# Kernel tuning notes

Measured on AMD Instinct MI355X. Metric: run time of the kernel, lower is better.

## Reference

```python
import jax, jax.numpy as jnp
import numpy as np

FRS = np.array([1, 2, 4, 8, 16, 25, 36, 50, 75], dtype=np.float32)
N_EXPERTS = len(FRS)
N = 1048576
DIMS = [(4, 32), (32, 32), (32, 64), (64, 64)]


def setup_inputs() -> dict:
    key = jax.random.key(0)
    ks = jax.random.split(key, 2 + 8)
    # features: col 0 = framerate drawn from the known framerate set, cols 1:5 = affinity feats
    fr_idx = jax.random.randint(ks[0], (N,), 0, N_EXPERTS)
    framerates = jnp.asarray(FRS)[fr_idx]
    aff = jax.random.normal(ks[1], (N, 4), dtype=jnp.float32)
    features = jnp.concatenate([framerates[:, None], aff], axis=1)
    # stacked per-expert MLP params (torch Linear: y = x @ W.T + b; store W as [in,out])
    params = {}
    scale = 0.1
    for li, (din, dout) in enumerate(DIMS):
        params[f"W{li+1}"] = scale * jax.random.normal(ks[2 + 2 * li], (N_EXPERTS, din, dout), dtype=jnp.float32)
        params[f"b{li+1}"] = scale * jax.random.normal(ks[3 + 2 * li], (N_EXPERTS, dout), dtype=jnp.float32)
    return {"features": features, **params}


def _expert_mlp(x, W1, b1, W2, b2, W3, b3, W4, b4):
    h = jax.nn.relu(x @ W1 + b1)
    h = jax.nn.relu(h @ W2 + b2)
    h = jax.nn.relu(h @ W3 + b3)
    return h @ W4 + b4  # [N, 64]


def reference(features, W1, b1, W2, b2, W3, b3, W4, b4):
    frs = jnp.asarray(FRS)
    framerates = features[:, 0]
    x = features[:, 1:]  # [N, 4] (ignore_appr=False)
    # nearest-framerate expert index (argmin picks first min, matching find_index)
    k = jnp.argmin(jnp.abs(framerates[:, None] - frs[None, :]), axis=1)  # [N]
    pred = jnp.zeros(features.shape[0], dtype=features.dtype)
    for e in range(N_EXPERTS):  # fixed, small expert set
        out_e = _expert_mlp(x, W1[e], b1[e], W2[e], b2[e], W3[e], b3[e], W4[e], b4[e])
        pred = jnp.where(k == e, out_e.sum(axis=1), pred)
    return pred
```

## Files before the change

### kernel.cpp

```cpp
#include <hip/hip_runtime.h>
#include <stdint.h>

#define NEXP 9
#define FTHR 512
#define RPH 4
#define SBLK (FTHR * RPH)
#define PADSLK (SBLK + NEXP * 32)
#define MAXT 80
#define TBL_BYTES 7936
#define CLS_STRIDE 168

typedef float f32x4 __attribute__((ext_vector_type(4)));
typedef float f32x16 __attribute__((ext_vector_type(16)));
typedef _Float16 f16x8 __attribute__((ext_vector_type(8)));

struct alignas(16) I4 { int a, b, c, d; };
struct alignas(64) Q4 { f32x4 a, b, c, d; };

__device__ __forceinline__ int pk(float a, float b) {
    return __builtin_bit_cast(int, __builtin_amdgcn_cvt_pkrtz(a, b));
}
__device__ __forceinline__ f32x16 zero16() {
    f32x16 z;
#pragma unroll
    for (int r = 0; r < 16; ++r) z[r] = 0.f;
    return z;
}

__device__ __forceinline__ int expert_of(float fr) {
    const float frs[NEXP] = {1.f, 2.f, 4.f, 8.f, 16.f, 25.f, 36.f, 50.f, 75.f};
    int k = 0;
    float best = fabsf(fr - frs[0]);
#pragma unroll
    for (int e = 1; e < NEXP; ++e) {
        float d = fabsf(fr - frs[e]);
        if (d < best) { best = d; k = e; }
    }
    return k;
}

__global__ __launch_bounds__(256) void k_prep(const float* __restrict__ W1, const float* __restrict__ b1,
                                              const float* __restrict__ W2, const float* __restrict__ b2,
                                              const float* __restrict__ W3, const float* __restrict__ b3,
                                              const float* __restrict__ W4, const float* __restrict__ b4,
                                              char* __restrict__ tab) {
    int e = blockIdx.x;
    int tid = threadIdx.x;
    char* T = tab + (size_t)e * TBL_BYTES;

    __shared__ float psum[64][4];
    __shared__ float rs2[64];
    __shared__ float b4s_s;
    {
        int row = tid >> 2, q = tid & 3;
        const float* w = W4 + (size_t)e * 4096 + row * 64 + q * 16;
        f32x4 a = *(const f32x4*)(w + 0), b = *(const f32x4*)(w + 4);
        f32x4 c = *(const f32x4*)(w + 8), d = *(const f32x4*)(w + 12);
        psum[row][q] = (a.x + a.y + a.z + a.w) + (b.x + b.y + b.z + b.w)
                     + (c.x + c.y + c.z + c.w) + (d.x + d.y + d.z + d.w);
    }
    __syncthreads();
    if (tid < 64) {
        int l = tid, g = l >> 5, m = l & 31;
        rs2[l] = psum[l][0] + psum[l][1] + psum[l][2] + psum[l][3];
        float bp = b4[e * 64 + l];
#pragma unroll
        for (int d = 1; d < 64; d <<= 1) bp += __shfl_xor(bp, d, 64);
        if (l == 0) b4s_s = bp;

        {
            f16x8 v;
#pragma unroll
            for (int ei = 0; ei < 8; ++ei) {
                int k = g * 8 + ei;
                float w = (k < 4) ? W1[e * 128 + k * 32 + m] : (k == 4 ? b1[e * 32 + m] : 0.f);
                v[ei] = (_Float16)w;
            }
            *(f16x8*)(T + 0 * 1024 + l * 16) = v;
        }
#pragma unroll
        for (int kf = 0; kf < 2; ++kf) {
            f16x8 v;
#pragma unroll
            for (int ei = 0; ei < 8; ++ei) {
                int row = kf * 16 + (ei & 3) + 8 * (ei >> 2) + 4 * g;
                v[ei] = (_Float16)W2[e * 1024 + row * 32 + m];
            }
            *(f16x8*)(T + (1 + kf) * 1024 + l * 16) = v;
        }
#pragma unroll
        for (int t = 0; t < 2; ++t)
#pragma unroll
            for (int kf = 0; kf < 2; ++kf) {
                f16x8 v;
#pragma unroll
                for (int ei = 0; ei < 8; ++ei) {
                    int row = kf * 16 + (ei & 3) + 8 * (ei >> 2) + 4 * g;
                    v[ei] = (_Float16)W3[e * 2048 + row * 64 + t * 32 + m];
                }
                *(f16x8*)(T + (3 + t * 2 + kf) * 1024 + l * 16) = v;
            }
    }
    __syncthreads();
    if (tid < 32) {
        int g = tid >> 4, r = tid & 15;
        int row = (r & 3) + 8 * (r >> 2) + 4 * g;
        float* C = (float*)(T + 7168);
        C[0 * 32 + tid] = b2[e * 32 + row];
        C[1 * 32 + tid] = b3[e * 64 + row];
        C[2 * 32 + tid] = b3[e * 64 + 32 + row];
        C[3 * 32 + tid] = rs2[row];
        C[4 * 32 + tid] = rs2[32 + row];
        if (tid == 0) C[160] = b4s_s;
    }
}

__global__ __launch_bounds__(FTHR, 4) void k_main(const float* __restrict__ feat, int n,
                                                  const char* __restrict__ tab,
                                                  float* __restrict__ out) {
    __shared__ uint2 bx[PADSLK];
    __shared__ unsigned short bidx[PADSLK];
    __shared__ float cls[NEXP * CLS_STRIDE];
    __shared__ int lcnt[NEXP];
    __shared__ int pbase[NEXP];
    __shared__ int wbase[RPH][8][NEXP];
    __shared__ unsigned char tile_e[MAXT];
    __shared__ short tile_s[MAXT];
    __shared__ unsigned char tile_v[MAXT];
    __shared__ int nt_s;

    int bid = blockIdx.x, tid = threadIdx.x;
    int wid = tid >> 6, lane = tid & 63, g = lane >> 5, m = lane & 31;
    int gbase = bid * SBLK;

    if (tid < NEXP) lcnt[tid] = 0;
    {
        uint2 z = {0u, 0u};
#pragma unroll
        for (int q = 0; q < 5; ++q) {
            int o = q * FTHR + tid;
            if (o < PADSLK) bx[o] = z;
        }
    }
    {
        const float* tf = (const float*)tab;
        for (int idx = tid; idx < NEXP * 161; idx += FTHR) {
            int e = idx / 161, o = idx - e * 161;
            cls[e * CLS_STRIDE + o] = tf[e * (TBL_BYTES / 4) + 1792 + o];
        }
    }
    __syncthreads();

    int kk[RPH], rk[RPH];
    uint2 xw[RPH];
#pragma unroll
    for (int r = 0; r < RPH; ++r) {
        int i = gbase + r * FTHR + tid;
        int k = -1;
        uint2 w = {0u, 0u};
        if (i < n) {
            const float* f = feat + (size_t)i * 5;
            k = expert_of(f[0]);
            w.x = (unsigned)pk(f[1], f[2]);
            w.y = (unsigned)pk(f[3], f[4]);
        }
        kk[r] = k; xw[r] = w;
        unsigned long long myM = 0;
#pragma unroll
        for (int e = 0; e < NEXP; ++e) {
            unsigned long long mm = __ballot(k == e);
            if (k == e) myM = mm;
            if (lane == 0) {
                int c = __popcll(mm);
                wbase[r][wid][e] = c ? atomicAdd(&lcnt[e], c) : 0;
            }
        }
        rk[r] = __popcll(myM & ((1ull << lane) - 1ull));
    }
    __syncthreads();

    if (wid == 0) {
        int e = lane;
        int c = (e < NEXP) ? lcnt[e] : 0;
        int ntl = (c + 31) >> 5;
        int padc = ntl << 5;
        int sp = padc, st = ntl;
#pragma unroll
        for (int d = 1; d < 16; d <<= 1) {
            int a = __shfl_up(sp, d, 64);
            int b = __shfl_up(st, d, 64);
            if (lane >= d) { sp += a; st += b; }
        }
        if (e < NEXP) {
            int pb = sp - padc, tb = st - ntl;
            pbase[e] = pb;
            for (int j = 0; j < ntl; ++j) {
                tile_e[tb + j] = (unsigned char)e;
                tile_s[tb + j] = (short)(pb + j * 32);
                int v = c - j * 32;
                tile_v[tb + j] = (unsigned char)(v > 32 ? 32 : v);
            }
            if (e == NEXP - 1) nt_s = st;
        }
    }
    __syncthreads();

#pragma unroll
    for (int r = 0; r < RPH; ++r) {
        int k = kk[r];
        if (k >= 0) {
            int slot = pbase[k] + wbase[r][wid][k] + rk[r];
            bx[slot] = xw[r];
            bidx[slot] = (unsigned short)(r * FTHR + tid);
        }
    }
    __syncthreads();

    int nt = nt_s;
    int t0 = (wid * nt) >> 3, t1 = ((wid + 1) * nt) >> 3;
    int cur_e = -1;
    f16x8 A1 = {}, A2a = {}, A2b = {}, A30a = {}, A30b = {}, A31a = {}, A31b = {};
    f32x16 W40r = zero16(), W41r = zero16();
    float b4v = 0.f;
    const float* Cc = cls;
    for (int t = t0; t < t1; ++t) {
        int e = __builtin_amdgcn_readfirstlane((int)tile_e[t]);
        if (e != cur_e) {
            cur_e = e;
            const char* T = tab + (size_t)e * TBL_BYTES;
            A1 = *(const f16x8*)(T + 0 * 1024 + lane * 16);
            A2a = *(const f16x8*)(T + 1 * 1024 + lane * 16);
            A2b = *(const f16x8*)(T + 2 * 1024 + lane * 16);
            A30a = *(const f16x8*)(T + 3 * 1024 + lane * 16);
            A30b = *(const f16x8*)(T + 4 * 1024 + lane * 16);
            A31a = *(const f16x8*)(T + 5 * 1024 + lane * 16);
            A31b = *(const f16x8*)(T + 6 * 1024 + lane * 16);
            Cc = cls + e * CLS_STRIDE + g * 16;
            {
                Q4 q;
                const float* c = Cc + 3 * 32;
                q.a = *(const f32x4*)(c + 0); q.b = *(const f32x4*)(c + 4);
                q.c = *(const f32x4*)(c + 8); q.d = *(const f32x4*)(c + 12);
                W40r = __builtin_bit_cast(f32x16, q);
                const float* c2 = Cc + 4 * 32;
                q.a = *(const f32x4*)(c2 + 0); q.b = *(const f32x4*)(c2 + 4);
                q.c = *(const f32x4*)(c2 + 8); q.d = *(const f32x4*)(c2 + 12);
                W41r = __builtin_bit_cast(f32x16, q);
            }
            b4v = cls[e * CLS_STRIDE + 160];
        }
        auto ldC = [&](int mat) -> f32x16 {
            const float* c = Cc + mat * 32;
            Q4 q;
            q.a = *(const f32x4*)(c + 0);
            q.b = *(const f32x4*)(c + 4);
            q.c = *(const f32x4*)(c + 8);
            q.d = *(const f32x4*)(c + 12);
            return __builtin_bit_cast(f32x16, q);
        };

        int s = tile_s[t], v = tile_v[t];
        uint2 xv = bx[s + m];

        I4 b1i = {g ? 0 : (int)xv.x, g ? 0 : (int)xv.y, g ? 0 : 0x3C00, 0};
        f16x8 B1 = __builtin_bit_cast(f16x8, b1i);

        f32x16 d1 = __builtin_amdgcn_mfma_f32_32x32x16_f16(A1, B1, zero16(), 0, 0, 0);
#pragma unroll
        for (int r = 0; r < 16; ++r) d1[r] = fmaxf(d1[r], 0.f);
        I4 p0 = {pk(d1[0], d1[1]), pk(d1[2], d1[3]), pk(d1[4], d1[5]), pk(d1[6], d1[7])};
        I4 p1 = {pk(d1[8], d1[9]), pk(d1[10], d1[11]), pk(d1[12], d1[13]), pk(d1[14], d1[15])};
        f16x8 B2a = __builtin_bit_cast(f16x8, p0);
        f16x8 B2b = __builtin_bit_cast(f16x8, p1);

        f32x16 d2 = __builtin_amdgcn_mfma_f32_32x32x16_f16(A2a, B2a, ldC(0), 0, 0, 0);
        d2 = __builtin_amdgcn_mfma_f32_32x32x16_f16(A2b, B2b, d2, 0, 0, 0);
#pragma unroll
        for (int r = 0; r < 16; ++r) d2[r] = fmaxf(d2[r], 0.f);
        I4 q0 = {pk(d2[0], d2[1]), pk(d2[2], d2[3]), pk(d2[4], d2[5]), pk(d2[6], d2[7])};
        I4 q1 = {pk(d2[8], d2[9]), pk(d2[10], d2[11]), pk(d2[12], d2[13]), pk(d2[14], d2[15])};
        f16x8 B3a = __builtin_bit_cast(f16x8, q0);
        f16x8 B3b = __builtin_bit_cast(f16x8, q1);

        float acc = 0.f;
        {
            f32x16 d3 = __builtin_amdgcn_mfma_f32_32x32x16_f16(A30a, B3a, ldC(1), 0, 0, 0);
            d3 = __builtin_amdgcn_mfma_f32_32x32x16_f16(A30b, B3b, d3, 0, 0, 0);
#pragma unroll
            for (int r = 0; r < 16; ++r) acc += fmaxf(d3[r], 0.f) * W40r[r];
        }
        {
            f32x16 d3 = __builtin_amdgcn_mfma_f32_32x32x16_f16(A31a, B3a, ldC(2), 0, 0, 0);
            d3 = __builtin_amdgcn_mfma_f32_32x32x16_f16(A31b, B3b, d3, 0, 0, 0);
#pragma unroll
            for (int r = 0; r < 16; ++r) acc += fmaxf(d3[r], 0.f) * W41r[r];
        }
        acc += __shfl_xor(acc, 32, 64);
        float rres = acc + b4v;
        if (!g && m < v) out[gbase + (int)bidx[s + m]] = rres;
    }
}

__global__ __launch_bounds__(256) void k_fallback(const float* __restrict__ feat,
                                                  const float* __restrict__ W1, const float* __restrict__ b1,
                                                  const float* __restrict__ W2, const float* __restrict__ b2,
                                                  const float* __restrict__ W3, const float* __restrict__ b3,
                                                  const float* __restrict__ W4, const float* __restrict__ b4,
                                                  float* __restrict__ out, int n) {
    int i = blockIdx.x * 256 + threadIdx.x;
    if (i >= n) return;
    const float* f = feat + (size_t)i * 5;
    int e = expert_of(f[0]);
    float x0 = f[1], x1 = f[2], x2 = f[3], x3 = f[4];
    float h1[32], h2[32], h3[64];
    for (int j = 0; j < 32; ++j) {
        float a = b1[e * 32 + j];
        a += x0 * W1[e * 128 + 0 * 32 + j];
        a += x1 * W1[e * 128 + 1 * 32 + j];
        a += x2 * W1[e * 128 + 2 * 32 + j];
        a += x3 * W1[e * 128 + 3 * 32 + j];
        h1[j] = fmaxf(a, 0.f);
    }
    for (int j = 0; j < 32; ++j) h2[j] = b2[e * 32 + j];
    for (int i2 = 0; i2 < 32; ++i2)
        for (int j = 0; j < 32; ++j) h2[j] += h1[i2] * W2[e * 1024 + i2 * 32 + j];
    for (int j = 0; j < 32; ++j) h2[j] = fmaxf(h2[j], 0.f);
    for (int j = 0; j < 64; ++j) h3[j] = b3[e * 64 + j];
    for (int i2 = 0; i2 < 32; ++i2)
        for (int j = 0; j < 64; ++j) h3[j] += h2[i2] * W3[e * 2048 + i2 * 64 + j];
    float pred = 0.f;
    for (int o = 0; o < 64; ++o) pred += b4[e * 64 + o];
    for (int j = 0; j < 64; ++j) {
        float rsum = 0.f;
        for (int o = 0; o < 64; ++o) rsum += W4[e * 4096 + j * 64 + o];
        pred += fmaxf(h3[j], 0.f) * rsum;
    }
    out[i] = pred;
}

extern "C" void kernel_launch(void* const* d_in, const int* in_sizes, int n_in,
                              void* d_out, int out_size, void* d_ws, size_t ws_size,
                              hipStream_t stream) {
    const float* feat = (const float*)d_in[0];
    const float* W1 = (const float*)d_in[1];
    const float* b1 = (const float*)d_in[2];
    const float* W2 = (const float*)d_in[3];
    const float* b2 = (const float*)d_in[4];
    const float* W3 = (const float*)d_in[5];
    const float* b3 = (const float*)d_in[6];
    const float* W4 = (const float*)d_in[7];
    const float* b4 = (const float*)d_in[8];
    float* out = (float*)d_out;
    int n = in_sizes[0] / 5;

    const size_t need = (size_t)NEXP * TBL_BYTES;

    if (ws_size >= need) {
        char* tab = (char*)d_ws;
        k_prep<<<NEXP, 256, 0, stream>>>(W1, b1, W2, b2, W3, b3, W4, b4, tab);
        int nb = (n + SBLK - 1) / SBLK;
        k_main<<<nb, FTHR, 0, stream>>>(feat, n, tab, out);
    } else {
        k_fallback<<<(n + 255) / 256, 256, 0, stream>>>(feat, W1, b1, W2, b2, W3, b3, W4, b4, out, n);
    }
}
```

Baseline: 33.55 us.

## Fuse weight-prep into main kernel and pack weights per block on the fly

```diff
diff --git a/kernel.cpp b/kernel.cpp
--- a/kernel.cpp
+++ b/kernel.cpp
@@ -7,8 +7,7 @@
 #define SBLK (FTHR * RPH)
 #define PADSLK (SBLK + NEXP * 32)
 #define MAXT 80
-#define TBL_BYTES 7936
-#define CLS_STRIDE 168
+#define CTS 168
 
 typedef float f32x4 __attribute__((ext_vector_type(4)));
 typedef float f32x16 __attribute__((ext_vector_type(16)));
@@ -20,6 +19,13 @@
 __device__ __forceinline__ int pk(float a, float b) {
     return __builtin_bit_cast(int, __builtin_amdgcn_cvt_pkrtz(a, b));
 }
+__device__ __forceinline__ int pkh(float a, float b) {
+    int p = pk(a, b);
+    int r;
+    int z = 0;
+    asm("v_pk_max_f16 %0, %1, %2" : "=v"(r) : "v"(p), "v"(z));
+    return r;
+}
 __device__ __forceinline__ f32x16 zero16() {
     f32x16 z;
 #pragma unroll
@@ -28,102 +34,24 @@
 }
 
 __device__ __forceinline__ int expert_of(float fr) {
-    const float frs[NEXP] = {1.f, 2.f, 4.f, 8.f, 16.f, 25.f, 36.f, 50.f, 75.f};
-    int k = 0;
-    float best = fabsf(fr - frs[0]);
-#pragma unroll
-    for (int e = 1; e < NEXP; ++e) {
-        float d = fabsf(fr - frs[e]);
-        if (d < best) { best = d; k = e; }
-    }
-    return k;
-}
-
-__global__ __launch_bounds__(256) void k_prep(const float* __restrict__ W1, const float* __restrict__ b1,
+    return (fr > 1.5f) + (fr > 3.f) + (fr > 6.f) + (fr > 12.f)
+         + (fr > 20.5f) + (fr > 30.5f) + (fr > 43.f) + (fr > 62.5f);
+}
+
+__global__ __launch_bounds__(FTHR) void k_all(const float* __restrict__ feat, int n,
+                                              const float* __restrict__ W1, const float* __restrict__ b1,
                                               const float* __restrict__ W2, const float* __restrict__ b2,
                                               const float* __restrict__ W3, const float* __restrict__ b3,
                                               const float* __restrict__ W4, const float* __restrict__ b4,
-                                              char* __restrict__ tab) {
-    int e = blockIdx.x;
-    int tid = threadIdx.x;
-    char* T = tab + (size_t)e * TBL_BYTES;
-
-    __shared__ float psum[64][4];
-    __shared__ float rs2[64];
-    __shared__ float b4s_s;
-    {
-        int row = tid >> 2, q = tid & 3;
-        const float* w = W4 + (size_t)e * 4096 + row * 64 + q * 16;
-        f32x4 a = *(const f32x4*)(w + 0), b = *(const f32x4*)(w + 4);
-        f32x4 c = *(const f32x4*)(w + 8), d = *(const f32x4*)(w + 12);
-        psum[row][q] = (a.x + a.y + a.z + a.w) + (b.x + b.y + b.z + b.w)
-                     + (c.x + c.y + c.z + c.w) + (d.x + d.y + d.z + d.w);
-    }
-    __syncthreads();
-    if (tid < 64) {
-        int l = tid, g = l >> 5, m = l & 31;
-        rs2[l] = psum[l][0] + psum[l][1] + psum[l][2] + psum[l][3];
-        float bp = b4[e * 64 + l];
-#pragma unroll
-        for (int d = 1; d < 64; d <<= 1) bp += __shfl_xor(bp, d, 64);
-        if (l == 0) b4s_s = bp;
-
-        {
-            f16x8 v;
-#pragma unroll
-            for (int ei = 0; ei < 8; ++ei) {
-                int k = g * 8 + ei;
-                float w = (k < 4) ? W1[e * 128 + k * 32 + m] : (k == 4 ? b1[e * 32 + m] : 0.f);
-                v[ei] = (_Float16)w;
-            }
-            *(f16x8*)(T + 0 * 1024 + l * 16) = v;
-        }
-#pragma unroll
-        for (int kf = 0; kf < 2; ++kf) {
-            f16x8 v;
-#pragma unroll
-            for (int ei = 0; ei < 8; ++ei) {
-                int row = kf * 16 + (ei & 3) + 8 * (ei >> 2) + 4 * g;
-                v[ei] = (_Float16)W2[e * 1024 + row * 32 + m];
-            }
-            *(f16x8*)(T + (1 + kf) * 1024 + l * 16) = v;
-        }
-#pragma unroll
-        for (int t = 0; t < 2; ++t)
-#pragma unroll
-            for (int kf = 0; kf < 2; ++kf) {
-                f16x8 v;
-#pragma unroll
-                for (int ei = 0; ei < 8; ++ei) {
-                    int row = kf * 16 + (ei & 3) + 8 * (ei >> 2) + 4 * g;
-                    v[ei] = (_Float16)W3[e * 2048 + row * 64 + t * 32 + m];
-                }
-                *(f16x8*)(T + (3 + t * 2 + kf) * 1024 + l * 16) = v;
-            }
-    }
-    __syncthreads();
-    if (tid < 32) {
-        int g = tid >> 4, r = tid & 15;
-        int row = (r & 3) + 8 * (r >> 2) + 4 * g;
-        float* C = (float*)(T + 7168);
-        C[0 * 32 + tid] = b2[e * 32 + row];
-        C[1 * 32 + tid] = b3[e * 64 + row];
-        C[2 * 32 + tid] = b3[e * 64 + 32 + row];
-        C[3 * 32 + tid] = rs2[row];
-        C[4 * 32 + tid] = rs2[32 + row];
-        if (tid == 0) C[160] = b4s_s;
-    }
-}
-
-__global__ __launch_bounds__(FTHR, 4) void k_main(const float* __restrict__ feat, int n,
-                                                  const char* __restrict__ tab,
-                                                  float* __restrict__ out) {
-    __shared__ uint2 bx[PADSLK];
+                                              float* __restrict__ out) {
+    __shared__ __align__(16) uint2 bx[PADSLK];
     __shared__ unsigned short bidx[PADSLK];
-    __shared__ float cls[NEXP * CLS_STRIDE];
+    __shared__ __align__(16) float rs[NEXP * 64];
+    __shared__ __align__(16) float ct[NEXP * CTS];
+    __shared__ float tmp36[36];
     __shared__ int lcnt[NEXP];
     __shared__ int pbase[NEXP];
-    __shared__ int wbase[RPH][8][NEXP];
+    __shared__ int wcnt[RPH][8][NEXP];
     __shared__ unsigned char tile_e[MAXT];
     __shared__ short tile_s[MAXT];
     __shared__ unsigned char tile_v[MAXT];
@@ -134,21 +62,6 @@
     int gbase = bid * SBLK;
 
     if (tid < NEXP) lcnt[tid] = 0;
-    {
-        uint2 z = {0u, 0u};
-#pragma unroll
-        for (int q = 0; q < 5; ++q) {
-            int o = q * FTHR + tid;
-            if (o < PADSLK) bx[o] = z;
-        }
-    }
-    {
-        const float* tf = (const float*)tab;
-        for (int idx = tid; idx < NEXP * 161; idx += FTHR) {
-            int e = idx / 161, o = idx - e * 161;
-            cls[e * CLS_STRIDE + o] = tf[e * (TBL_BYTES / 4) + 1792 + o];
-        }
-    }
     __syncthreads();
 
     int kk[RPH], rk[RPH];
@@ -172,10 +85,41 @@
             if (k == e) myM = mm;
             if (lane == 0) {
                 int c = __popcll(mm);
-                wbase[r][wid][e] = c ? atomicAdd(&lcnt[e], c) : 0;
+                wcnt[r][wid][e] = c ? atomicAdd(&lcnt[e], c) : 0;
             }
         }
         rk[r] = __popcll(myM & ((1ull << lane) - 1ull));
+    }
+    for (int rr = tid; rr < NEXP * 64; rr += FTHR) {
+        int e = rr >> 6, row = rr & 63;
+        const float* w = W4 + (size_t)e * 4096 + row * 64;
+        f32x4 s4 = {0.f, 0.f, 0.f, 0.f};
+#pragma unroll
+        for (int q = 0; q < 16; ++q) s4 += *(const f32x4*)(w + q * 4);
+        rs[rr] = s4.x + s4.y + s4.z + s4.w;
+    }
+    if (tid < 36) {
+        int e = tid >> 2, q = tid & 3;
+        const float* bb = b4 + e * 64 + q * 16;
+        f32x4 s4 = {0.f, 0.f, 0.f, 0.f};
+#pragma unroll
+        for (int q2 = 0; q2 < 4; ++q2) s4 += *(const f32x4*)(bb + q2 * 4);
+        tmp36[tid] = s4.x + s4.y + s4.z + s4.w;
+    }
+    if (tid < NEXP * 32) {
+        int e = tid >> 5, idx = tid & 31, gg = idx >> 4, r = idx & 15;
+        int row = (r & 3) + 8 * (r >> 2) + 4 * gg;
+        ct[e * CTS + idx] = b2[e * 32 + row];
+        ct[e * CTS + 32 + idx] = b3[e * 64 + row];
+        ct[e * CTS + 64 + idx] = b3[e * 64 + 32 + row];
+    }
+    {
+        uint2 z = {0u, 0u};
+#pragma unroll
+        for (int q = 0; q < 5; ++q) {
+            int o = q * FTHR + tid;
+            if (o < PADSLK) bx[o] = z;
+        }
     }
     __syncthreads();
 
@@ -203,13 +147,24 @@
             if (e == NEXP - 1) nt_s = st;
         }
     }
+    if (tid >= 64 && tid < 64 + NEXP * 32) {
+        int t2 = tid - 64;
+        int e = t2 >> 5, idx = t2 & 31, gg = idx >> 4, r = idx & 15;
+        int base = (r & 3) + 8 * (r >> 2) + 4 * gg;
+        ct[e * CTS + 96 + idx] = rs[e * 64 + base];
+        ct[e * CTS + 128 + idx] = rs[e * 64 + 32 + base];
+    }
+    if (tid >= 384 && tid < 384 + NEXP) {
+        int e = tid - 384;
+        ct[e * CTS + 160] = tmp36[4 * e] + tmp36[4 * e + 1] + tmp36[4 * e + 2] + tmp36[4 * e + 3];
+    }
     __syncthreads();
 
 #pragma unroll
     for (int r = 0; r < RPH; ++r) {
         int k = kk[r];
         if (k >= 0) {
-            int slot = pbase[k] + wbase[r][wid][k] + rk[r];
+            int slot = pbase[k] + wcnt[r][wid][k] + rk[r];
             bx[slot] = xw[r];
             bidx[slot] = (unsigned short)(r * FTHR + tid);
         }
@@ -219,35 +174,65 @@
     int nt = nt_s;
     int t0 = (wid * nt) >> 3, t1 = ((wid + 1) * nt) >> 3;
     int cur_e = -1;
-    f16x8 A1 = {}, A2a = {}, A2b = {}, A30a = {}, A30b = {}, A31a = {}, A31b = {};
+    f16x8 A[7];
+#pragma unroll
+    for (int c = 0; c < 7; ++c) A[c] = f16x8{};
     f32x16 W40r = zero16(), W41r = zero16();
+    const float* Cc = ct;
     float b4v = 0.f;
-    const float* Cc = cls;
+
     for (int t = t0; t < t1; ++t) {
         int e = __builtin_amdgcn_readfirstlane((int)tile_e[t]);
         if (e != cur_e) {
             cur_e = e;
-            const char* T = tab + (size_t)e * TBL_BYTES;
-            A1 = *(const f16x8*)(T + 0 * 1024 + lane * 16);
-            A2a = *(const f16x8*)(T + 1 * 1024 + lane * 16);
-            A2b = *(const f16x8*)(T + 2 * 1024 + lane * 16);
-            A30a = *(const f16x8*)(T + 3 * 1024 + lane * 16);
-            A30b = *(const f16x8*)(T + 4 * 1024 + lane * 16);
-            A31a = *(const f16x8*)(T + 5 * 1024 + lane * 16);
-            A31b = *(const f16x8*)(T + 6 * 1024 + lane * 16);
-            Cc = cls + e * CLS_STRIDE + g * 16;
+            const float* w1 = W1 + e * 128;
+            const float* w2 = W2 + (size_t)e * 1024;
+            const float* w3 = W3 + (size_t)e * 2048;
+            {
+                I4 av = {0, 0, 0, 0};
+                if (!g) {
+                    av.a = pk(w1[0 * 32 + m], w1[1 * 32 + m]);
+                    av.b = pk(w1[2 * 32 + m], w1[3 * 32 + m]);
+                    av.c = pk(b1[e * 32 + m], 0.f);
+                }
+                A[0] = __builtin_bit_cast(f16x8, av);
+            }
+#pragma unroll
+            for (int kf = 0; kf < 2; ++kf) {
+                int rb = kf * 16 + 4 * g;
+                I4 av;
+                av.a = pk(w2[(rb + 0) * 32 + m], w2[(rb + 1) * 32 + m]);
+                av.b = pk(w2[(rb + 2) * 32 + m], w2[(rb + 3) * 32 + m]);
+                av.c = pk(w2[(rb + 8) * 32 + m], w2[(rb + 9) * 32 + m]);
+                av.d = pk(w2[(rb + 10) * 32 + m], w2[(rb + 11) * 32 + m]);
+                A[1 + kf] = __builtin_bit_cast(f16x8, av);
+            }
+#pragma unroll
+            for (int t2 = 0; t2 < 2; ++t2)
+#pragma unroll
+                for (int kf = 0; kf < 2; ++kf) {
+                    int rb = kf * 16 + 4 * g;
+                    int cm = t2 * 32 + m;
+                    I4 av;
+                    av.a = pk(w3[(rb + 0) * 64 + cm], w3[(rb + 1) * 64 + cm]);
+                    av.b = pk(w3[(rb + 2) * 64 + cm], w3[(rb + 3) * 64 + cm]);
+                    av.c = pk(w3[(rb + 8) * 64 + cm], w3[(rb + 9) * 64 + cm]);
+                    av.d = pk(w3[(rb + 10) * 64 + cm], w3[(rb + 11) * 64 + cm]);
+                    A[3 + t2 * 2 + kf] = __builtin_bit_cast(f16x8, av);
+                }
+            Cc = ct + e * CTS + g * 16;
             {
                 Q4 q;
-                const float* c = Cc + 3 * 32;
+                const float* c = Cc + 96;
                 q.a = *(const f32x4*)(c + 0); q.b = *(const f32x4*)(c + 4);
                 q.c = *(const f32x4*)(c + 8); q.d = *(const f32x4*)(c + 12);
                 W40r = __builtin_bit_cast(f32x16, q);
-                const float* c2 = Cc + 4 * 32;
+                const float* c2 = Cc + 128;
                 q.a = *(const f32x4*)(c2 + 0); q.b = *(const f32x4*)(c2 + 4);
                 q.c = *(const f32x4*)(c2 + 8); q.d = *(const f32x4*)(c2 + 12);
                 W41r = __builtin_bit_cast(f32x16, q);
             }
-            b4v = cls[e * CLS_STRIDE + 160];
+            b4v = ct[e * CTS + 160];
         }
         auto ldC = [&](int mat) -> f32x16 {
             const float* c = Cc + mat * 32;
@@ -265,77 +250,35 @@
         I4 b1i = {g ? 0 : (int)xv.x, g ? 0 : (int)xv.y, g ? 0 : 0x3C00, 0};
         f16x8 B1 = __builtin_bit_cast(f16x8, b1i);
 
-        f32x16 d1 = __builtin_amdgcn_mfma_f32_32x32x16_f16(A1, B1, zero16(), 0, 0, 0);
-#pragma unroll
-        for (int r = 0; r < 16; ++r) d1[r] = fmaxf(d1[r], 0.f);
-        I4 p0 = {pk(d1[0], d1[1]), pk(d1[2], d1[3]), pk(d1[4], d1[5]), pk(d1[6], d1[7])};
-        I4 p1 = {pk(d1[8], d1[9]), pk(d1[10], d1[11]), pk(d1[12], d1[13]), pk(d1[14], d1[15])};
+        f32x16 d1 = __builtin_amdgcn_mfma_f32_32x32x16_f16(A[0], B1, zero16(), 0, 0, 0);
+        I4 p0 = {pkh(d1[0], d1[1]), pkh(d1[2], d1[3]), pkh(d1[4], d1[5]), pkh(d1[6], d1[7])};
+        I4 p1 = {pkh(d1[8], d1[9]), pkh(d1[10], d1[11]), pkh(d1[12], d1[13]), pkh(d1[14], d1[15])};
         f16x8 B2a = __builtin_bit_cast(f16x8, p0);
         f16x8 B2b = __builtin_bit_cast(f16x8, p1);
 
-        f32x16 d2 = __builtin_amdgcn_mfma_f32_32x32x16_f16(A2a, B2a, ldC(0), 0, 0, 0);
-        d2 = __builtin_amdgcn_mfma_f32_32x32x16_f16(A2b, B2b, d2, 0, 0, 0);
-#pragma unroll
-        for (int r = 0; r < 16; ++r) d2[r] = fmaxf(d2[r], 0.f);
-        I4 q0 = {pk(d2[0], d2[1]), pk(d2[2], d2[3]), pk(d2[4], d2[5]), pk(d2[6], d2[7])};
-        I4 q1 = {pk(d2[8], d2[9]), pk(d2[10], d2[11]), pk(d2[12], d2[13]), pk(d2[14], d2[15])};
+        f32x16 d2 = __builtin_amdgcn_mfma_f32_32x32x16_f16(A[1], B2a, ldC(0), 0, 0, 0);
+        d2 = __builtin_amdgcn_mfma_f32_32x32x16_f16(A[2], B2b, d2, 0, 0, 0);
+        I4 q0 = {pkh(d2[0], d2[1]), pkh(d2[2], d2[3]), pkh(d2[4], d2[5]), pkh(d2[6], d2[7])};
+        I4 q1 = {pkh(d2[8], d2[9]), pkh(d2[10], d2[11]), pkh(d2[12], d2[13]), pkh(d2[14], d2[15])};
         f16x8 B3a = __builtin_bit_cast(f16x8, q0);
         f16x8 B3b = __builtin_bit_cast(f16x8, q1);
 
         float acc = 0.f;
         {
-            f32x16 d3 = __builtin_amdgcn_mfma_f32_32x32x16_f16(A30a, B3a, ldC(1), 0, 0, 0);
-            d3 = __builtin_amdgcn_mfma_f32_32x32x16_f16(A30b, B3b, d3, 0, 0, 0);
+            f32x16 d3 = __builtin_amdgcn_mfma_f32_32x32x16_f16(A[3], B3a, ldC(1), 0, 0, 0);
+            d3 = __builtin_amdgcn_mfma_f32_32x32x16_f16(A[4], B3b, d3, 0, 0, 0);
 #pragma unroll
             for (int r = 0; r < 16; ++r) acc += fmaxf(d3[r], 0.f) * W40r[r];
         }
         {
-            f32x16 d3 = __builtin_amdgcn_mfma_f32_32x32x16_f16(A31a, B3a, ldC(2), 0, 0, 0);
-            d3 = __builtin_amdgcn_mfma_f32_32x32x16_f16(A31b, B3b, d3, 0, 0, 0);
+            f32x16 d3 = __builtin_amdgcn_mfma_f32_32x32x16_f16(A[5], B3a, ldC(2), 0, 0, 0);
+            d3 = __builtin_amdgcn_mfma_f32_32x32x16_f16(A[6], B3b, d3, 0, 0, 0);
 #pragma unroll
             for (int r = 0; r < 16; ++r) acc += fmaxf(d3[r], 0.f) * W41r[r];
         }
         acc += __shfl_xor(acc, 32, 64);
-        float rres = acc + b4v;
-        if (!g && m < v) out[gbase + (int)bidx[s + m]] = rres;
-    }
-}
-
-__global__ __launch_bounds__(256) void k_fallback(const float* __restrict__ feat,
-                                                  const float* __restrict__ W1, const float* __restrict__ b1,
-                                                  const float* __restrict__ W2, const float* __restrict__ b2,
-                                                  const float* __restrict__ W3, const float* __restrict__ b3,
-                                                  const float* __restrict__ W4, const float* __restrict__ b4,
-                                                  float* __restrict__ out, int n) {
-    int i = blockIdx.x * 256 + threadIdx.x;
-    if (i >= n) return;
-    const float* f = feat + (size_t)i * 5;
-    int e = expert_of(f[0]);
-    float x0 = f[1], x1 = f[2], x2 = f[3], x3 = f[4];
-    float h1[32], h2[32], h3[64];
-    for (int j = 0; j < 32; ++j) {
-        float a = b1[e * 32 + j];
-        a += x0 * W1[e * 128 + 0 * 32 + j];
-        a += x1 * W1[e * 128 + 1 * 32 + j];
-        a += x2 * W1[e * 128 + 2 * 32 + j];
-        a += x3 * W1[e * 128 + 3 * 32 + j];
-        h1[j] = fmaxf(a, 0.f);
-    }
-    for (int j = 0; j < 32; ++j) h2[j] = b2[e * 32 + j];
-    for (int i2 = 0; i2 < 32; ++i2)
-        for (int j = 0; j < 32; ++j) h2[j] += h1[i2] * W2[e * 1024 + i2 * 32 + j];
-    for (int j = 0; j < 32; ++j) h2[j] = fmaxf(h2[j], 0.f);
-    for (int j = 0; j < 64; ++j) h3[j] = b3[e * 64 + j];
-    for (int i2 = 0; i2 < 32; ++i2)
-        for (int j = 0; j < 64; ++j) h3[j] += h2[i2] * W3[e * 2048 + i2 * 64 + j];
-    float pred = 0.f;
-    for (int o = 0; o < 64; ++o) pred += b4[e * 64 + o];
-    for (int j = 0; j < 64; ++j) {
-        float rsum = 0.f;
-        for (int o = 0; o < 64; ++o) rsum += W4[e * 4096 + j * 64 + o];
-        pred += fmaxf(h3[j], 0.f) * rsum;
-    }
-    out[i] = pred;
+        if (!g && m < v) out[gbase + (int)bidx[s + m]] = acc + b4v;
+    }
 }
 
 extern "C" void kernel_launch(void* const* d_in, const int* in_sizes, int n_in,
@@ -353,14 +296,6 @@
     float* out = (float*)d_out;
     int n = in_sizes[0] / 5;
 
-    const size_t need = (size_t)NEXP * TBL_BYTES;
-
-    if (ws_size >= need) {
-        char* tab = (char*)d_ws;
-        k_prep<<<NEXP, 256, 0, stream>>>(W1, b1, W2, b2, W3, b3, W4, b4, tab);
-        int nb = (n + SBLK - 1) / SBLK;
-        k_main<<<nb, FTHR, 0, stream>>>(feat, n, tab, out);
-    } else {
-        k_fallback<<<(n + 255) / 256, 256, 0, stream>>>(feat, W1, b1, W2, b2, W3, b3, W4, b4, out, n);
-    }
-}
+    int nb = (n + SBLK - 1) / SBLK;
+    k_all<<<nb, FTHR, 0, stream>>>(feat, n, W1, b1, W2, b2, W3, b3, W4, b4, out);
+}
```

After: 45.24 us. 1.35x slower.
